# Kernel optimization log

Hardware: AMD Instinct MI355X
Metric: run time of the kernel (lower is better)

Reference implementation:

```python
import jax, jax.numpy as jnp
import numpy as np

N_NODES = 100000
N_EDGES = 3200000
IN_DIM, HID, OUT = 5, 64, 2


def _gcn_conv(x, W, b, src, dst):
    """PyG GCNConv: out = D^-1/2 (A + I) D^-1/2 (x W) + b.
    src/dst are edge_index[0]/edge_index[1] (source_to_target flow)."""
    n = x.shape[0]
    h = x @ W  # [N, out]
    # degree including self loop: deg[i] = 1 + #edges with dst == i
    deg = jnp.ones((n,), h.dtype).at[dst].add(1.0)
    inv_sqrt = jax.lax.rsqrt(deg)
    coef = inv_sqrt[src] * inv_sqrt[dst]  # [E]
    msgs = h[src] * coef[:, None]  # [E, out] gather
    agg = jax.ops.segment_sum(msgs, dst, num_segments=n)  # scatter-add
    # self-loop contribution: norm = inv_sqrt[i]^2 = 1/deg[i]
    agg = agg + h * (1.0 / deg)[:, None]
    return agg + b


def setup_inputs() -> dict:
    key = jax.random.key(0)
    ks = jax.random.split(key, 8)
    x = jax.random.normal(ks[0], (N_NODES, IN_DIM), dtype=jnp.float32)
    edge_index = jax.random.randint(ks[1], (2, N_EDGES), 0, N_NODES, dtype=jnp.int32)
    def glorot(k, fan_in, fan_out):
        lim = np.sqrt(6.0 / (fan_in + fan_out)).astype(np.float32)
        return jax.random.uniform(k, (fan_in, fan_out), jnp.float32, -lim, lim)
    return {
        "x": x,
        "edge_index": edge_index,
        "W1": glorot(ks[2], IN_DIM, HID), "b1": jnp.zeros((HID,), jnp.float32),
        "W2": glorot(ks[3], HID, HID),    "b2": jnp.zeros((HID,), jnp.float32),
        "W3": glorot(ks[4], HID, OUT),    "b3": jnp.zeros((OUT,), jnp.float32),
    }


def reference(x, edge_index, W1, b1, W2, b2, W3, b3):
    src, dst = edge_index[0], edge_index[1]
    # eval mode: dropout is identity
    h = jax.nn.relu(_gcn_conv(x, W1, b1, src, dst))
    h = jax.nn.relu(_gcn_conv(h, W2, b2, src, dst))
    return _gcn_conv(h, W3, b3, src, dst)
```

## Files before the change

### kernel.cpp

```cpp
#include <hip/hip_runtime.h>

#define CB 256
#define MAXNB 1024


__global__ void k_hist(const int* __restrict__ dst, int* __restrict__ histG,
                       int E, int NB, int chunk) {
  __shared__ int hist[MAXNB];
  int b = blockIdx.x, tid = threadIdx.x;
  for (int k = tid; k < NB; k += 256) hist[k] = 0;
  __syncthreads();
  int beg = b * chunk, end = min(E, beg + chunk);
  for (int i = beg + tid; i < end; i += 256) atomicAdd(&hist[dst[i] >> 8], 1);
  __syncthreads();
  for (int k = tid; k < NB; k += 256) histG[(size_t)k * CB + b] = hist[k];
}

__global__ void k_scan_local(const int* __restrict__ in, int* __restrict__ out,
                             int* __restrict__ blockSums, int n) {
  __shared__ int wsum[16];
  __shared__ int wpre[16];
  int tid = threadIdx.x;
  int gid = blockIdx.x * 1024 + tid;
  int v = (gid < n) ? in[gid] : 0;
  int lane = tid & 63, wv = tid >> 6;
  int x = v;
#pragma unroll
  for (int d = 1; d < 64; d <<= 1) {
    int t = __shfl_up(x, d);
    if (lane >= d) x += t;
  }
  if (lane == 63) wsum[wv] = x;
  __syncthreads();
  if (tid == 0) {
    int run = 0;
#pragma unroll
    for (int i = 0; i < 16; ++i) { wpre[i] = run; run += wsum[i]; }
    blockSums[blockIdx.x] = run;
  }
  __syncthreads();
  if (gid < n) out[gid] = x - v + wpre[wv];
}

__global__ void k_scan_blocks(const int* __restrict__ blockSums, int* __restrict__ blockOffs, int nb) {
  if (threadIdx.x == 0 && blockIdx.x == 0) {
    int run = 0;
    for (int i = 0; i < nb; ++i) { blockOffs[i] = run; run += blockSums[i]; }
    blockOffs[nb] = run;
  }
}

__global__ void k_scan_addg(int* __restrict__ data, const int* __restrict__ blockOffs, int n) {
  int gid = blockIdx.x * 1024 + threadIdx.x;
  if (gid < n) data[gid] += blockOffs[blockIdx.x];
}

__global__ void k_scatter(const int* __restrict__ src, const int* __restrict__ dst,
                          const int* __restrict__ histS, unsigned* __restrict__ recs,
                          int E, int NB, int chunk) {
  __shared__ int cur[MAXNB];
  int b = blockIdx.x, tid = threadIdx.x;
  for (int k = tid; k < NB; k += 256) cur[k] = histS[(size_t)k * CB + b];
  __syncthreads();
  int beg = b * chunk, end = min(E, beg + chunk);
  for (int i = beg + tid; i < end; i += 256) {
    int s = src[i], d = dst[i];
    int pos = atomicAdd(&cur[d >> 8], 1);
    recs[pos] = ((unsigned)s << 8) | (unsigned)(d & 255);
  }
}

__global__ void k_build(const unsigned* __restrict__ recs, const int* __restrict__ histS,
                        int* __restrict__ offs, float* __restrict__ inv_sqrt,
                        int* __restrict__ srcs, int N, int NB, int E) {
  __shared__ int cnt[256];
  __shared__ int cur[256];
  __shared__ int wtot[4];
  int k = blockIdx.x, tid = threadIdx.x;
  int ebeg = histS[(size_t)k * CB];
  int eend = (k + 1 < NB) ? histS[(size_t)(k + 1) * CB] : E;
  cnt[tid] = 0;
  __syncthreads();
  for (int i = ebeg + tid; i < eend; i += 256) atomicAdd(&cnt[recs[i] & 255u], 1);
  __syncthreads();
  int v = cnt[tid];
  int lane = tid & 63, w = tid >> 6;
  int x = v;
#pragma unroll
  for (int d = 1; d < 64; d <<= 1) {
    int t = __shfl_up(x, d);
    if (lane >= d) x += t;
  }
  if (lane == 63) wtot[w] = x;
  __syncthreads();
  int pre = 0;
  for (int i = 0; i < w; ++i) pre += wtot[i];
  int gpos = ebeg + (x - v) + pre;
  int node = k * 256 + tid;
  if (node < N) {
    offs[node] = gpos;
    inv_sqrt[node] = rsqrtf(1.0f + (float)v);
  }
  cur[tid] = gpos;
  if (k == NB - 1 && tid == 0) offs[N] = E;
  __syncthreads();
  for (int i = ebeg + tid; i < eend; i += 256) {
    unsigned r = recs[i];
    int pos = atomicAdd(&cur[r & 255u], 1);
    srcs[pos] = (int)(r >> 8);
  }
}


__global__ void k_l12(const float* __restrict__ x, const int* __restrict__ offs,
                      const int* __restrict__ srcs, const float* __restrict__ inv_sqrt,
                      const float* __restrict__ W1, const float* __restrict__ b1,
                      const float* __restrict__ W2, float* __restrict__ h2raw, int n) {
  __shared__ float hrow[4 * 64];
  int tid = threadIdx.x;
  int lane = tid & 63, w = tid >> 6;
  float w1r[5];
#pragma unroll
  for (int k = 0; k < 5; ++k) w1r[k] = W1[k * 64 + lane];
  float bias = b1[lane];
  float wreg[64];
#pragma unroll
  for (int k = 0; k < 64; ++k) wreg[k] = W2[k * 64 + lane];
  float* slot = &hrow[w * 64];
  int wid0 = (blockIdx.x * blockDim.x + tid) >> 6;
  int nw = (gridDim.x * blockDim.x) >> 6;
  for (int i = wid0; i < n; i += nw) {
    int beg = offs[i], end = offs[i + 1];
    float isd = inv_sqrt[i];
    float a0 = 0.f, a1 = 0.f, a2 = 0.f, a3 = 0.f, a4 = 0.f;
    for (int j = beg + lane; j < end; j += 64) {
      int s = srcs[j];
      float c = inv_sqrt[s] * isd;
      const float* xs = x + (size_t)s * 5;
      a0 = fmaf(xs[0], c, a0); a1 = fmaf(xs[1], c, a1); a2 = fmaf(xs[2], c, a2);
      a3 = fmaf(xs[3], c, a3); a4 = fmaf(xs[4], c, a4);
    }
#pragma unroll
    for (int d = 32; d; d >>= 1) {
      a0 += __shfl_xor(a0, d); a1 += __shfl_xor(a1, d); a2 += __shfl_xor(a2, d);
      a3 += __shfl_xor(a3, d); a4 += __shfl_xor(a4, d);
    }
    float sc = isd * isd;
    const float* xi = x + (size_t)i * 5;
    a0 = fmaf(xi[0], sc, a0); a1 = fmaf(xi[1], sc, a1); a2 = fmaf(xi[2], sc, a2);
    a3 = fmaf(xi[3], sc, a3); a4 = fmaf(xi[4], sc, a4);
    float h1v = bias;
    h1v = fmaf(a0, w1r[0], h1v); h1v = fmaf(a1, w1r[1], h1v); h1v = fmaf(a2, w1r[2], h1v);
    h1v = fmaf(a3, w1r[3], h1v); h1v = fmaf(a4, w1r[4], h1v);
    h1v = fmaxf(h1v, 0.f);
    slot[lane] = h1v;
    float acc0 = 0.f, acc1 = 0.f, acc2 = 0.f, acc3 = 0.f;
#pragma unroll
    for (int k4 = 0; k4 < 16; ++k4) {
      float4 hq = *(const float4*)&slot[k4 * 4];
      acc0 = fmaf(hq.x, wreg[k4 * 4],     acc0);
      acc1 = fmaf(hq.y, wreg[k4 * 4 + 1], acc1);
      acc2 = fmaf(hq.z, wreg[k4 * 4 + 2], acc2);
      acc3 = fmaf(hq.w, wreg[k4 * 4 + 3], acc3);
    }
    h2raw[(size_t)i * 64 + lane] = (acc0 + acc1) + (acc2 + acc3);
  }
}

__global__ void k_agg64w3(const float* __restrict__ hraw, const int* __restrict__ offs,
                          const int* __restrict__ srcs, const float* __restrict__ inv_sqrt,
                          const float* __restrict__ b2, const float* __restrict__ W3,
                          float* __restrict__ h3, int n) {
  int wid = (blockIdx.x * blockDim.x + threadIdx.x) >> 6;
  int lane = threadIdx.x & 63;
  if (wid >= n) return;
  int sub = lane >> 4;
  int fl  = lane & 15;
  float w30[4], w31[4];
#pragma unroll
  for (int q = 0; q < 4; ++q) {
    w30[q] = W3[(fl * 4 + q) * 2];
    w31[q] = W3[(fl * 4 + q) * 2 + 1];
  }
  int beg = offs[wid], end = offs[wid + 1];
  float isd = inv_sqrt[wid];
  float ax0 = 0.f, ay0 = 0.f, az0 = 0.f, aw0 = 0.f;
  float ax1 = 0.f, ay1 = 0.f, az1 = 0.f, aw1 = 0.f;
  int j = beg + sub;
  for (; j + 12 < end; j += 16) {
    int s0 = srcs[j], s1 = srcs[j + 4], s2 = srcs[j + 8], s3 = srcs[j + 12];
    float c0 = inv_sqrt[s0] * isd, c1 = inv_sqrt[s1] * isd;
    float c2 = inv_sqrt[s2] * isd, c3 = inv_sqrt[s3] * isd;
    float4 r0 = *(const float4*)(hraw + (size_t)s0 * 64 + fl * 4);
    float4 r1 = *(const float4*)(hraw + (size_t)s1 * 64 + fl * 4);
    float4 r2 = *(const float4*)(hraw + (size_t)s2 * 64 + fl * 4);
    float4 r3 = *(const float4*)(hraw + (size_t)s3 * 64 + fl * 4);
    ax0 = fmaf(r0.x, c0, ax0); ay0 = fmaf(r0.y, c0, ay0);
    az0 = fmaf(r0.z, c0, az0); aw0 = fmaf(r0.w, c0, aw0);
    ax1 = fmaf(r1.x, c1, ax1); ay1 = fmaf(r1.y, c1, ay1);
    az1 = fmaf(r1.z, c1, az1); aw1 = fmaf(r1.w, c1, aw1);
    ax0 = fmaf(r2.x, c2, ax0); ay0 = fmaf(r2.y, c2, ay0);
    az0 = fmaf(r2.z, c2, az0); aw0 = fmaf(r2.w, c2, aw0);
    ax1 = fmaf(r3.x, c3, ax1); ay1 = fmaf(r3.y, c3, ay1);
    az1 = fmaf(r3.z, c3, az1); aw1 = fmaf(r3.w, c3, aw1);
  }
  for (; j < end; j += 4) {
    int s0 = srcs[j];
    float c0 = inv_sqrt[s0] * isd;
    float4 r0 = *(const float4*)(hraw + (size_t)s0 * 64 + fl * 4);
    ax0 = fmaf(r0.x, c0, ax0); ay0 = fmaf(r0.y, c0, ay0);
    az0 = fmaf(r0.z, c0, az0); aw0 = fmaf(r0.w, c0, aw0);
  }
  float ax = ax0 + ax1, ay = ay0 + ay1, az = az0 + az1, aw = aw0 + aw1;
  ax += __shfl_xor(ax, 16); ay += __shfl_xor(ay, 16);
  az += __shfl_xor(az, 16); aw += __shfl_xor(aw, 16);
  ax += __shfl_xor(ax, 32); ay += __shfl_xor(ay, 32);
  az += __shfl_xor(az, 32); aw += __shfl_xor(aw, 32);
  float sc = isd * isd;
  float4 self = *(const float4*)(hraw + (size_t)wid * 64 + fl * 4);
  float4 bb   = *(const float4*)(b2 + fl * 4);
  float hx = fmaxf(ax + self.x * sc + bb.x, 0.f);
  float hy = fmaxf(ay + self.y * sc + bb.y, 0.f);
  float hz = fmaxf(az + self.z * sc + bb.z, 0.f);
  float hw = fmaxf(aw + self.w * sc + bb.w, 0.f);
  float p0 = hx * w30[0] + hy * w30[1] + hz * w30[2] + hw * w30[3];
  float p1 = hx * w31[0] + hy * w31[1] + hz * w31[2] + hw * w31[3];
#pragma unroll
  for (int d = 8; d; d >>= 1) { p0 += __shfl_xor(p0, d); p1 += __shfl_xor(p1, d); }
  if (lane == 0) {
    h3[(size_t)wid * 2]     = p0;
    h3[(size_t)wid * 2 + 1] = p1;
  }
}

__global__ void k_agg2(const float* __restrict__ h3, const int* __restrict__ offs,
                       const int* __restrict__ srcs, const float* __restrict__ inv_sqrt,
                       const float* __restrict__ b3, float* __restrict__ out, int n) {
  int wid = (blockIdx.x * blockDim.x + threadIdx.x) >> 6;
  int lane = threadIdx.x & 63;
  if (wid >= n) return;
  int beg = offs[wid], end = offs[wid + 1];
  float isd = inv_sqrt[wid];
  float a0 = 0.f, a1 = 0.f;
  for (int j = beg + lane; j < end; j += 64) {
    int s = srcs[j];
    float c = inv_sqrt[s] * isd;
    a0 = fmaf(h3[(size_t)s * 2], c, a0);
    a1 = fmaf(h3[(size_t)s * 2 + 1], c, a1);
  }
#pragma unroll
  for (int d = 32; d; d >>= 1) { a0 += __shfl_xor(a0, d); a1 += __shfl_xor(a1, d); }
  if (lane == 0) {
    float sc = isd * isd;
    out[(size_t)wid * 2]     = a0 + h3[(size_t)wid * 2] * sc + b3[0];
    out[(size_t)wid * 2 + 1] = a1 + h3[(size_t)wid * 2 + 1] * sc + b3[1];
  }
}


extern "C" void kernel_launch(void* const* d_in, const int* in_sizes, int n_in,
                              void* d_out, int out_size, void* d_ws, size_t ws_size,
                              hipStream_t stream) {
  const float* x  = (const float*)d_in[0];
  const int*   ei = (const int*)d_in[1];
  const float* W1 = (const float*)d_in[2];
  const float* b1 = (const float*)d_in[3];
  const float* W2 = (const float*)d_in[4];
  const float* b2 = (const float*)d_in[5];
  const float* W3 = (const float*)d_in[6];
  const float* b3 = (const float*)d_in[7];
  float* out = (float*)d_out;

  const int N = in_sizes[0] / 5;
  const int E = in_sizes[1] / 2;
  const int* src = ei;
  const int* dst = ei + E;

  const int NB = (N + 255) >> 8;
  const int chunk = (E + CB - 1) / CB;
  const int n2 = NB * CB;
  const int nb2 = (n2 + 1023) / 1024;

  char* p = (char*)d_ws;
  auto alloc = [&](size_t bytes) {
    char* r = p;
    p += (bytes + 255) & ~(size_t)255;
    return r;
  };
  int*      histG     = (int*)alloc((size_t)n2 * 4);
  int*      histS     = (int*)alloc((size_t)n2 * 4);
  int*      blockSums = (int*)alloc((size_t)nb2 * 4);
  int*      blockOffs = (int*)alloc((size_t)(nb2 + 1) * 4);
  unsigned* recs      = (unsigned*)alloc((size_t)E * 4);
  int*      srcs      = (int*)alloc((size_t)E * 4);
  int*      offs      = (int*)alloc((size_t)(N + 1) * 4);
  float*    inv_sqrt  = (float*)alloc((size_t)N * 4);
  float*    hB        = (float*)alloc((size_t)N * 64 * 4);
  float*    h3        = (float*)alloc((size_t)N * 2 * 4);

  const int wavesBlocks = (N * 64 + 255) / 256;

  k_hist<<<CB, 256, 0, stream>>>(dst, histG, E, NB, chunk);
  k_scan_local<<<nb2, 1024, 0, stream>>>(histG, histS, blockSums, n2);
  k_scan_blocks<<<1, 64, 0, stream>>>(blockSums, blockOffs, nb2);
  k_scan_addg<<<nb2, 1024, 0, stream>>>(histS, blockOffs, n2);
  k_scatter<<<CB, 256, 0, stream>>>(src, dst, histS, recs, E, NB, chunk);
  k_build<<<NB, 256, 0, stream>>>(recs, histS, offs, inv_sqrt, srcs, N, NB, E);

  k_l12<<<2048, 256, 0, stream>>>(x, offs, srcs, inv_sqrt, W1, b1, W2, hB, N);
  k_agg64w3<<<wavesBlocks, 256, 0, stream>>>(hB, offs, srcs, inv_sqrt, b2, W3, h3, N);
  k_agg2<<<wavesBlocks, 256, 0, stream>>>(h3, offs, srcs, inv_sqrt, b3, out, N);
}
```

Baseline: 275.6 us.

## Parallelize block-offset scan, fold add-back into consumers, split waves across two nodes

```diff
diff --git a/kernel.cpp b/kernel.cpp
--- a/kernel.cpp
+++ b/kernel.cpp
@@ -43,24 +43,34 @@
 }
 
 __global__ void k_scan_blocks(const int* __restrict__ blockSums, int* __restrict__ blockOffs, int nb) {
-  if (threadIdx.x == 0 && blockIdx.x == 0) {
-    int run = 0;
-    for (int i = 0; i < nb; ++i) { blockOffs[i] = run; run += blockSums[i]; }
-    blockOffs[nb] = run;
-  }
-}
-
-__global__ void k_scan_addg(int* __restrict__ data, const int* __restrict__ blockOffs, int n) {
-  int gid = blockIdx.x * 1024 + threadIdx.x;
-  if (gid < n) data[gid] += blockOffs[blockIdx.x];
+  __shared__ int wtot[4];
+  int tid = threadIdx.x;
+  int lane = tid & 63, w = tid >> 6;
+  int v = (tid < nb) ? blockSums[tid] : 0;
+  int x = v;
+#pragma unroll
+  for (int d = 1; d < 64; d <<= 1) {
+    int t = __shfl_up(x, d);
+    if (lane >= d) x += t;
+  }
+  if (lane == 63) wtot[w] = x;
+  __syncthreads();
+  int pre = 0;
+  for (int i = 0; i < w; ++i) pre += wtot[i];
+  int ex = x - v + pre;
+  if (tid < nb) blockOffs[tid] = ex;
+  if (tid == nb - 1) blockOffs[nb] = ex + v;
 }
 
 __global__ void k_scatter(const int* __restrict__ src, const int* __restrict__ dst,
-                          const int* __restrict__ histS, unsigned* __restrict__ recs,
-                          int E, int NB, int chunk) {
+                          const int* __restrict__ histS, const int* __restrict__ blockOffs,
+                          unsigned* __restrict__ recs, int E, int NB, int chunk) {
   __shared__ int cur[MAXNB];
   int b = blockIdx.x, tid = threadIdx.x;
-  for (int k = tid; k < NB; k += 256) cur[k] = histS[(size_t)k * CB + b];
+  for (int k = tid; k < NB; k += 256) {
+    int gid = k * CB + b;
+    cur[k] = histS[gid] + blockOffs[gid >> 10];
+  }
   __syncthreads();
   int beg = b * chunk, end = min(E, beg + chunk);
   for (int i = beg + tid; i < end; i += 256) {
@@ -71,14 +81,20 @@
 }
 
 __global__ void k_build(const unsigned* __restrict__ recs, const int* __restrict__ histS,
+                        const int* __restrict__ blockOffs,
                         int* __restrict__ offs, float* __restrict__ inv_sqrt,
                         int* __restrict__ srcs, int N, int NB, int E) {
   __shared__ int cnt[256];
   __shared__ int cur[256];
   __shared__ int wtot[4];
   int k = blockIdx.x, tid = threadIdx.x;
-  int ebeg = histS[(size_t)k * CB];
-  int eend = (k + 1 < NB) ? histS[(size_t)(k + 1) * CB] : E;
+  int g0 = k * CB;
+  int ebeg = histS[g0] + blockOffs[g0 >> 10];
+  int eend = E;
+  if (k + 1 < NB) {
+    int g1 = (k + 1) * CB;
+    eend = histS[g1] + blockOffs[g1 >> 10];
+  }
   cnt[tid] = 0;
   __syncthreads();
   for (int i = ebeg + tid; i < eend; i += 256) atomicAdd(&cnt[recs[i] & 255u], 1);
@@ -116,9 +132,10 @@
                       const int* __restrict__ srcs, const float* __restrict__ inv_sqrt,
                       const float* __restrict__ W1, const float* __restrict__ b1,
                       const float* __restrict__ W2, float* __restrict__ h2raw, int n) {
-  __shared__ float hrow[4 * 64];
+  __shared__ float hrow[4][2][64];
   int tid = threadIdx.x;
   int lane = tid & 63, w = tid >> 6;
+  int hl = lane & 31, half = lane >> 5;
   float w1r[5];
 #pragma unroll
   for (int k = 0; k < 5; ++k) w1r[k] = W1[k * 64 + lane];
@@ -126,44 +143,76 @@
   float wreg[64];
 #pragma unroll
   for (int k = 0; k < 64; ++k) wreg[k] = W2[k * 64 + lane];
-  float* slot = &hrow[w * 64];
+  float* slotA = &hrow[w][0][0];
+  float* slotB = &hrow[w][1][0];
   int wid0 = (blockIdx.x * blockDim.x + tid) >> 6;
   int nw = (gridDim.x * blockDim.x) >> 6;
-  for (int i = wid0; i < n; i += nw) {
-    int beg = offs[i], end = offs[i + 1];
-    float isd = inv_sqrt[i];
+  for (int i2 = wid0 * 2; i2 < n; i2 += nw * 2) {
+    int iA = i2, iB = i2 + 1;
+    int node = (half == 0) ? iA : iB;
+    bool valid = node < n;
     float a0 = 0.f, a1 = 0.f, a2 = 0.f, a3 = 0.f, a4 = 0.f;
-    for (int j = beg + lane; j < end; j += 64) {
-      int s = srcs[j];
-      float c = inv_sqrt[s] * isd;
-      const float* xs = x + (size_t)s * 5;
-      a0 = fmaf(xs[0], c, a0); a1 = fmaf(xs[1], c, a1); a2 = fmaf(xs[2], c, a2);
-      a3 = fmaf(xs[3], c, a3); a4 = fmaf(xs[4], c, a4);
-    }
-#pragma unroll
-    for (int d = 32; d; d >>= 1) {
+    float isd = 0.f;
+    if (valid) {
+      isd = inv_sqrt[node];
+      int beg = offs[node], end = offs[node + 1];
+      for (int j = beg + hl; j < end; j += 32) {
+        int s = srcs[j];
+        float c = inv_sqrt[s] * isd;
+        const float* xs = x + (size_t)s * 5;
+        float4 xv = *(const float4*)xs;
+        float x4 = xs[4];
+        a0 = fmaf(xv.x, c, a0); a1 = fmaf(xv.y, c, a1); a2 = fmaf(xv.z, c, a2);
+        a3 = fmaf(xv.w, c, a3); a4 = fmaf(x4, c, a4);
+      }
+    }
+#pragma unroll
+    for (int d = 16; d; d >>= 1) {
       a0 += __shfl_xor(a0, d); a1 += __shfl_xor(a1, d); a2 += __shfl_xor(a2, d);
       a3 += __shfl_xor(a3, d); a4 += __shfl_xor(a4, d);
     }
-    float sc = isd * isd;
-    const float* xi = x + (size_t)i * 5;
-    a0 = fmaf(xi[0], sc, a0); a1 = fmaf(xi[1], sc, a1); a2 = fmaf(xi[2], sc, a2);
-    a3 = fmaf(xi[3], sc, a3); a4 = fmaf(xi[4], sc, a4);
-    float h1v = bias;
-    h1v = fmaf(a0, w1r[0], h1v); h1v = fmaf(a1, w1r[1], h1v); h1v = fmaf(a2, w1r[2], h1v);
-    h1v = fmaf(a3, w1r[3], h1v); h1v = fmaf(a4, w1r[4], h1v);
-    h1v = fmaxf(h1v, 0.f);
-    slot[lane] = h1v;
-    float acc0 = 0.f, acc1 = 0.f, acc2 = 0.f, acc3 = 0.f;
+    if (valid) {
+      float sc = isd * isd;
+      const float* xi = x + (size_t)node * 5;
+      a0 = fmaf(xi[0], sc, a0); a1 = fmaf(xi[1], sc, a1); a2 = fmaf(xi[2], sc, a2);
+      a3 = fmaf(xi[3], sc, a3); a4 = fmaf(xi[4], sc, a4);
+    }
+    float aA0 = __shfl(a0, hl),      aA1 = __shfl(a1, hl),      aA2 = __shfl(a2, hl);
+    float aA3 = __shfl(a3, hl),      aA4 = __shfl(a4, hl);
+    float aB0 = __shfl(a0, hl | 32), aB1 = __shfl(a1, hl | 32), aB2 = __shfl(a2, hl | 32);
+    float aB3 = __shfl(a3, hl | 32), aB4 = __shfl(a4, hl | 32);
+    float hA = bias;
+    hA = fmaf(aA0, w1r[0], hA); hA = fmaf(aA1, w1r[1], hA); hA = fmaf(aA2, w1r[2], hA);
+    hA = fmaf(aA3, w1r[3], hA); hA = fmaf(aA4, w1r[4], hA);
+    hA = fmaxf(hA, 0.f);
+    float hB = bias;
+    hB = fmaf(aB0, w1r[0], hB); hB = fmaf(aB1, w1r[1], hB); hB = fmaf(aB2, w1r[2], hB);
+    hB = fmaf(aB3, w1r[3], hB); hB = fmaf(aB4, w1r[4], hB);
+    hB = fmaxf(hB, 0.f);
+    slotA[lane] = hA;
+    slotB[lane] = hB;
+    float ac0 = 0.f, ac1 = 0.f, ac2 = 0.f, ac3 = 0.f;
 #pragma unroll
     for (int k4 = 0; k4 < 16; ++k4) {
-      float4 hq = *(const float4*)&slot[k4 * 4];
-      acc0 = fmaf(hq.x, wreg[k4 * 4],     acc0);
-      acc1 = fmaf(hq.y, wreg[k4 * 4 + 1], acc1);
-      acc2 = fmaf(hq.z, wreg[k4 * 4 + 2], acc2);
-      acc3 = fmaf(hq.w, wreg[k4 * 4 + 3], acc3);
-    }
-    h2raw[(size_t)i * 64 + lane] = (acc0 + acc1) + (acc2 + acc3);
+      float4 hq = *(const float4*)&slotA[k4 * 4];
+      ac0 = fmaf(hq.x, wreg[k4 * 4],     ac0);
+      ac1 = fmaf(hq.y, wreg[k4 * 4 + 1], ac1);
+      ac2 = fmaf(hq.z, wreg[k4 * 4 + 2], ac2);
+      ac3 = fmaf(hq.w, wreg[k4 * 4 + 3], ac3);
+    }
+    h2raw[(size_t)iA * 64 + lane] = (ac0 + ac1) + (ac2 + ac3);
+    if (iB < n) {
+      float bc0 = 0.f, bc1 = 0.f, bc2 = 0.f, bc3 = 0.f;
+#pragma unroll
+      for (int k4 = 0; k4 < 16; ++k4) {
+        float4 hq = *(const float4*)&slotB[k4 * 4];
+        bc0 = fmaf(hq.x, wreg[k4 * 4],     bc0);
+        bc1 = fmaf(hq.y, wreg[k4 * 4 + 1], bc1);
+        bc2 = fmaf(hq.z, wreg[k4 * 4 + 2], bc2);
+        bc3 = fmaf(hq.w, wreg[k4 * 4 + 3], bc3);
+      }
+      h2raw[(size_t)iB * 64 + lane] = (bc0 + bc1) + (bc2 + bc3);
+    }
   }
 }
 
@@ -302,10 +351,9 @@
 
   k_hist<<<CB, 256, 0, stream>>>(dst, histG, E, NB, chunk);
   k_scan_local<<<nb2, 1024, 0, stream>>>(histG, histS, blockSums, n2);
-  k_scan_blocks<<<1, 64, 0, stream>>>(blockSums, blockOffs, nb2);
-  k_scan_addg<<<nb2, 1024, 0, stream>>>(histS, blockOffs, n2);
-  k_scatter<<<CB, 256, 0, stream>>>(src, dst, histS, recs, E, NB, chunk);
-  k_build<<<NB, 256, 0, stream>>>(recs, histS, offs, inv_sqrt, srcs, N, NB, E);
+  k_scan_blocks<<<1, 256, 0, stream>>>(blockSums, blockOffs, nb2);
+  k_scatter<<<CB, 256, 0, stream>>>(src, dst, histS, blockOffs, recs, E, NB, chunk);
+  k_build<<<NB, 256, 0, stream>>>(recs, histS, blockOffs, offs, inv_sqrt, srcs, N, NB, E);
 
   k_l12<<<2048, 256, 0, stream>>>(x, offs, srcs, inv_sqrt, W1, b1, W2, hB, N);
   k_agg64w3<<<wavesBlocks, 256, 0, stream>>>(hB, offs, srcs, inv_sqrt, b2, W3, h3, N);
```

After: 263.7 us. 1.05x faster.
